# Kernel optimization log

Hardware: AMD Instinct MI355X
Metric: run time of the kernel (lower is better)

The kernel has to match this reference:

```python
import jax, jax.numpy as jnp
import numpy as np

B, S, HID = 1, 2048, 2048
NUM_HEADS, NUM_KV_HEADS, HEAD_DIM = 16, 4, 128
ROPE_THETA = 10000.0
EPS = 1e-6


def setup_inputs() -> dict:
    key = jax.random.key(0)
    ks = jax.random.split(key, 9)
    s = 0.02
    return {
        "hidden_states": jax.random.normal(ks[0], (B, S, HID), jnp.float32),
        "mu_prev": jax.random.normal(ks[1], (B, S, HID), jnp.float32),
        "wq": jax.random.normal(ks[2], (NUM_HEADS * HEAD_DIM, HID), jnp.float32) * s,
        "wk": jax.random.normal(ks[3], (NUM_KV_HEADS * HEAD_DIM, HID), jnp.float32) * s,
        "wv": jax.random.normal(ks[4], (NUM_KV_HEADS * HEAD_DIM, HID), jnp.float32) * s,
        "wo": jax.random.normal(ks[5], (HID, NUM_HEADS * HEAD_DIM), jnp.float32) * s,
        "wmq": jax.random.normal(ks[6], (NUM_HEADS * HEAD_DIM, HID), jnp.float32) * (s * 0.1),
        "wmk": jax.random.normal(ks[7], (NUM_KV_HEADS * HEAD_DIM, HID), jnp.float32) * (s * 0.1),
        "wmv": jax.random.normal(ks[8], (NUM_KV_HEADS * HEAD_DIM, HID), jnp.float32) * (s * 0.1),
        "q_norm_w": jnp.ones((HEAD_DIM,), jnp.float32),
        "k_norm_w": jnp.ones((HEAD_DIM,), jnp.float32),
    }


def _rmsnorm(x, w):
    var = jnp.mean(jnp.square(x), axis=-1, keepdims=True)
    return x * jax.lax.rsqrt(var + EPS) * w


def _rope_cos_sin(seq_len, dtype):
    inv_freq = 1.0 / (ROPE_THETA ** (jnp.arange(0, HEAD_DIM, 2, dtype=jnp.float32) / HEAD_DIM))
    freqs = jnp.arange(seq_len, dtype=jnp.float32)[:, None] * inv_freq[None, :]  # [S, D/2]
    emb = jnp.concatenate([freqs, freqs], axis=-1)  # [S, D]
    return jnp.cos(emb).astype(dtype), jnp.sin(emb).astype(dtype)


def _rotate_half(x):
    x1, x2 = jnp.split(x, 2, axis=-1)
    return jnp.concatenate([-x2, x1], axis=-1)


def reference(hidden_states, mu_prev, wq, wk, wv, wo, wmq, wmk, wmv, q_norm_w, k_norm_w):
    b, s, _ = hidden_states.shape
    # Fused mu-guided QKV projections (cat(x, mu) @ cat(W, Wm)^T == x@W^T + mu@Wm^T)
    q = hidden_states @ wq.T + mu_prev @ wmq.T  # [B,S,H*D]
    k = hidden_states @ wk.T + mu_prev @ wmk.T  # [B,S,KV*D]
    v = hidden_states @ wv.T + mu_prev @ wmv.T
    q = q.reshape(b, s, NUM_HEADS, HEAD_DIM).transpose(0, 2, 1, 3)      # [B,H,S,D]
    k = k.reshape(b, s, NUM_KV_HEADS, HEAD_DIM).transpose(0, 2, 1, 3)   # [B,KV,S,D]
    v = v.reshape(b, s, NUM_KV_HEADS, HEAD_DIM).transpose(0, 2, 1, 3)
    # per-head QK RMSNorm
    q = _rmsnorm(q, q_norm_w)
    k = _rmsnorm(k, k_norm_w)
    # RoPE
    cos, sin = _rope_cos_sin(s, q.dtype)
    q = q * cos + _rotate_half(q) * sin
    k = k * cos + _rotate_half(k) * sin
    # GQA attention without materializing repeated K/V: group query heads
    g = NUM_HEADS // NUM_KV_HEADS
    qg = q.reshape(b, NUM_KV_HEADS, g, s, HEAD_DIM)
    scale = 1.0 / jnp.sqrt(jnp.asarray(HEAD_DIM, q.dtype))
    scores = jnp.einsum('bkgqd,bkld->bkgql', qg, k) * scale  # [B,KV,G,S,S]
    causal = jnp.tril(jnp.ones((s, s), bool))
    scores = jnp.where(causal, scores, jnp.asarray(-jnp.inf, scores.dtype))
    probs = jax.nn.softmax(scores.astype(jnp.float32), axis=-1).astype(q.dtype)
    out = jnp.einsum('bkgql,bkld->bkgqd', probs, v)  # [B,KV,G,S,D]
    out = out.reshape(b, NUM_HEADS, s, HEAD_DIM).transpose(0, 2, 1, 3).reshape(b, s, NUM_HEADS * HEAD_DIM)
    return out @ wo.T
```

## Files before the change

kernel.cpp:

```cpp
#include <hip/hip_runtime.h>
#include <math.h>

#define SEQ 2048
#define HID_DIM 2048
#define NH 16
#define NKV 4
#define HD 128
#define QS 3072

typedef float  f4v  __attribute__((ext_vector_type(4)));
typedef __bf16 bf8v __attribute__((ext_vector_type(8)));
typedef __bf16 bf4v __attribute__((ext_vector_type(4)));
typedef __bf16 bf2v __attribute__((ext_vector_type(2)));

typedef __attribute__((address_space(1))) const void* gvp;
typedef __attribute__((address_space(3))) void*       svp;

__device__ __forceinline__ void gld16(const void* g, void* lds_wave_base) {
    __builtin_amdgcn_global_load_lds((gvp)g, (svp)lds_wave_base, 16, 0, 0);
}

__device__ __forceinline__ void wgb() {
    asm volatile("" ::: "memory");
    __builtin_amdgcn_s_barrier();
    asm volatile("" ::: "memory");
}
#define VMC(n) asm volatile("s_waitcnt vmcnt(" #n ")" ::: "memory")

__global__ __launch_bounds__(256)
void cvt_cat2(__bf16* __restrict__ dst, const float* __restrict__ s0,
              const float* __restrict__ s1, int rows, int kq)
{
    int i = blockIdx.x * 256 + threadIdx.x;
    if (i >= rows * kq * 2) return;
    int row = i / (2 * kq), c = i - row * 2 * kq;
    const float* s = (c < kq) ? s0 + ((size_t)row * kq + c) * 4
                              : s1 + ((size_t)row * kq + (c - kq)) * 4;
    float4 v = *reinterpret_cast<const float4*>(s);
    *reinterpret_cast<bf4v*>(dst + ((size_t)row * 2 * kq + c) * 4) =
        bf4v{ (__bf16)v.x, (__bf16)v.y, (__bf16)v.z, (__bf16)v.w };
}

__global__ __launch_bounds__(256)
void cvt(__bf16* __restrict__ dst, const float* __restrict__ src, int n4)
{
    int i = blockIdx.x * 256 + threadIdx.x;
    if (i >= n4) return;
    float4 v = *reinterpret_cast<const float4*>(src + (size_t)i * 4);
    *reinterpret_cast<bf4v*>(dst + (size_t)i * 4) =
        bf4v{ (__bf16)v.x, (__bf16)v.y, (__bf16)v.z, (__bf16)v.w };
}

__device__ __forceinline__ void stage_half(
    const __bf16* __restrict__ g, int ldk, int row0, int ktile, int half,
    char* buf, int w, int sr, int sc)
{
#pragma unroll
    for (int j = 0; j < 2; ++j) {
        int sid = w * 2 + j;
        int rb = half * 8 + (sid >> 1), cb = sid & 1;
        gld16(g + (size_t)(row0 + rb * 16 + sr) * ldk + ktile * 64 + cb * 32 + sc,
              buf + (rb * 2 + cb) * 1024);
    }
}
__device__ __forceinline__ void stage_tile(
    const __bf16* __restrict__ g, int ldk, int row0, int ktile,
    char* buf, int w, int sr, int sc)
{
    stage_half(g, ldk, row0, ktile, 0, buf, w, sr, sc);
    stage_half(g, ldk, row0, ktile, 1, buf, w, sr, sc);
}

#define LOAD_AF(DST, BUF, MTB) \
    _Pragma("unroll") for (int mt = 0; mt < 4; ++mt) \
    _Pragma("unroll") for (int ks = 0; ks < 2; ++ks) \
        DST[mt][ks] = *(const bf8v*)((BUF) + (((wm * 8 + (MTB) + mt) * 2 + ks) << 10) + frag_off);
#define LOAD_BF(DST, BUF, NTB) \
    _Pragma("unroll") for (int nt = 0; nt < 2; ++nt) \
    _Pragma("unroll") for (int ks = 0; ks < 2; ++ks) \
        DST[nt][ks] = *(const bf8v*)((BUF) + (((wn * 4 + (NTB) + nt) * 2 + ks) << 10) + frag_off);
#define MFMA_Q(MTB, NTB, AR, BR) \
    __builtin_amdgcn_s_setprio(1); \
    _Pragma("unroll") for (int mt = 0; mt < 4; ++mt) \
    _Pragma("unroll") for (int nt = 0; nt < 2; ++nt) \
    _Pragma("unroll") for (int ks = 0; ks < 2; ++ks) \
        acc[(MTB) + mt][(NTB) + nt] = __builtin_amdgcn_mfma_f32_16x16x32_bf16( \
            AR[mt][ks], BR[nt][ks], acc[(MTB) + mt][(NTB) + nt], 0, 0, 0); \
    __builtin_amdgcn_s_setprio(0);

__global__ __launch_bounds__(512, 2)
void gemm_nt_pl(const __bf16* __restrict__ A, const __bf16* __restrict__ B,
                __bf16* __restrict__ P, int M, int N, int K, int KS)
{
    __shared__ __align__(1024) char lds[131072];
    char* A0 = lds;
    char* A1 = lds + 32768;
    char* B0 = lds + 65536;
    char* B1 = lds + 98304;

    const int tid = threadIdx.x, lane = tid & 63, w = tid >> 6;
    const int wm = w >> 2, wn = w & 3;
    const int mm = lane & 15, quad = lane >> 4;
    const int m0 = blockIdx.y * 256, n0 = blockIdx.x * 256;
    const int kt0 = (blockIdx.z * KS) >> 6;
    const int T = KS >> 6;

    const int sr = lane >> 2, sc = (lane & 3) * 8;
    const int frag_off = (mm * 4 + quad) << 4;

    f4v acc[8][4] = {};
    bf8v aLo[4][2], aHi[4][2], b01e[2][2], b01o[2][2], b23[2][2];

    stage_tile(A, K, m0, kt0,     A0, w, sr, sc);
    stage_tile(B, K, n0, kt0,     B0, w, sr, sc);
    stage_tile(A, K, m0, kt0 + 1, A1, w, sr, sc);
    stage_tile(B, K, n0, kt0 + 1, B1, w, sr, sc);
    VMC(8);
    wgb();
    LOAD_AF(aLo, A0, 0)
    LOAD_BF(b01e, B0, 0)

    const int nbody = (T - 2) >> 1;
    for (int it = 0; it < nbody; ++it) {
        const int t2 = kt0 + 2 * it + 2, t3 = t2 + 1;
        LOAD_BF(b23, B0, 2)
        MFMA_Q(0, 0, aLo, b01e)
        wgb();
        LOAD_AF(aHi, A0, 4)
        MFMA_Q(0, 2, aLo, b23)
        VMC(0);
        wgb();
        LOAD_AF(aLo, A1, 0)
        stage_tile(B, K, n0, t2, B0, w, sr, sc);
        MFMA_Q(4, 2, aHi, b23)
        wgb();
        LOAD_BF(b01o, B1, 0)
        stage_tile(A, K, m0, t2, A0, w, sr, sc);
        MFMA_Q(4, 0, aHi, b01e)
        wgb();
        LOAD_BF(b23, B1, 2)
        MFMA_Q(0, 0, aLo, b01o)
        wgb();
        LOAD_AF(aHi, A1, 4)
        MFMA_Q(0, 2, aLo, b23)
        VMC(0);
        wgb();
        LOAD_AF(aLo, A0, 0)
        stage_tile(B, K, n0, t3, B1, w, sr, sc);
        MFMA_Q(4, 2, aHi, b23)
        wgb();
        LOAD_BF(b01e, B0, 0)
        stage_tile(A, K, m0, t3, A1, w, sr, sc);
        MFMA_Q(4, 0, aHi, b01o)
        wgb();
    }
    LOAD_BF(b23, B0, 2)
    MFMA_Q(0, 0, aLo, b01e)
    wgb();
    LOAD_AF(aHi, A0, 4)
    MFMA_Q(0, 2, aLo, b23)
    VMC(0);
    wgb();
    LOAD_AF(aLo, A1, 0)
    MFMA_Q(4, 2, aHi, b23)
    wgb();
    LOAD_BF(b01o, B1, 0)
    MFMA_Q(4, 0, aHi, b01e)
    wgb();
    LOAD_BF(b23, B1, 2)
    MFMA_Q(0, 0, aLo, b01o)
    wgb();
    LOAD_AF(aHi, A1, 4)
    MFMA_Q(0, 2, aLo, b23)
    wgb();
    MFMA_Q(4, 2, aHi, b23)
    MFMA_Q(4, 0, aHi, b01o)

    __bf16* Pz = P + (size_t)blockIdx.z * M * N;
#pragma unroll
    for (int mt = 0; mt < 8; ++mt)
#pragma unroll
        for (int nt = 0; nt < 4; ++nt)
#pragma unroll
            for (int r = 0; r < 4; ++r)
                Pz[(size_t)(m0 + wm * 128 + mt * 16 + quad * 4 + r) * N
                   + n0 + wn * 64 + nt * 16 + mm] = (__bf16)acc[mt][nt][r];
}

__global__ __launch_bounds__(256)
void add4(const __bf16* __restrict__ P, float* __restrict__ out, int n4)
{
    int i = blockIdx.x * 256 + threadIdx.x;
    if (i >= n4) return;
    float4 s = {0.f, 0.f, 0.f, 0.f};
#pragma unroll
    for (int z = 0; z < 4; ++z) {
        bf4v v = *reinterpret_cast<const bf4v*>(P + (size_t)z * n4 * 4 + (size_t)i * 4);
        s.x += (float)v[0]; s.y += (float)v[1]; s.z += (float)v[2]; s.w += (float)v[3];
    }
    *reinterpret_cast<float4*>(out + (size_t)i * 4) = s;
}

__global__ __launch_bounds__(64)
void norm_rope(__bf16* __restrict__ qkv ,
               const __bf16* __restrict__ p1,
               const float* __restrict__ qw, const float* __restrict__ kw)
{
    const int s = blockIdx.x, hh = blockIdx.y, l = threadIdx.x;
    const float* wn; float scale; int off;
    if (hh < NH) { off = hh * HD;               wn = qw; scale = 0.08838834764831845f; }
    else         { off = 2048 + (hh - NH) * HD; wn = kw; scale = 1.0f; }
    __bf16* p = qkv + (size_t)s * QS + off;
    const __bf16* q1 = p1 + (size_t)s * QS + off;
    float x0 = (float)p[l]      + (float)q1[l];
    float x1 = (float)p[l + 64] + (float)q1[l + 64];
    float ss = x0 * x0 + x1 * x1;
#pragma unroll
    for (int o = 32; o; o >>= 1) ss += __shfl_xor(ss, o);
    float inv = rsqrtf(ss * (1.0f / 128.0f) + 1e-6f);
    x0 *= inv * wn[l];
    x1 *= inv * wn[l + 64];
    float invf = exp2f(-(float)l * (13.287712379549449f / 64.0f));
    float ang  = (float)s * invf;
    float c, sn;
    sincosf(ang, &sn, &c);
    p[l]      = (__bf16)((x0 * c - x1 * sn) * scale);
    p[l + 64] = (__bf16)((x1 * c + x0 * sn) * scale);
}

__global__ __launch_bounds__(256)
void pack_k(const __bf16* __restrict__ qkv, __bf16* __restrict__ Kt)
{
    const int kt = blockIdx.x, kh = blockIdx.y, t = threadIdx.x;
    char* tile = (char*)Kt + ((size_t)(kh * 32 + kt)) * 16384;
    const __bf16* src = qkv + 2048 + kh * HD;
#pragma unroll
    for (int i = 0; i < 4; ++i) {
        int cid = t * 4 + i;
        int key = cid >> 4, pc = cid & 15;
        int c = pc ^ (key & 15);
        bf8v v = *reinterpret_cast<const bf8v*>(src + (size_t)(kt * 64 + key) * QS + c * 8);
        *reinterpret_cast<bf8v*>(tile + cid * 16) = v;
    }
}

__global__ __launch_bounds__(256)
void pack_v(const __bf16* __restrict__ qkv0, const __bf16* __restrict__ qkv1,
            __bf16* __restrict__ Vt)
{
    const int kt = blockIdx.x, kh = blockIdx.y, t = threadIdx.x;
    char* tile = (char*)Vt + ((size_t)(kh * 32 + kt)) * 16384;
    const __bf16* s0 = qkv0 + 2560 + kh * HD;
    const __bf16* s1 = qkv1 + 2560 + kh * HD;
#pragma unroll
    for (int i = 0; i < 4; ++i) {
        int cid = t * 4 + i;
        int d = cid >> 3, kcp = cid & 7;
        int kc = kcp ^ (d & 7);
        size_t base = (size_t)(kt * 64 + kc * 8) * QS + d;
        __bf16 tmp[8];
#pragma unroll
        for (int j = 0; j < 8; ++j)
            tmp[j] = (__bf16)((float)s0[base + (size_t)j * QS] +
                              (float)s1[base + (size_t)j * QS]);
        *reinterpret_cast<bf8v*>(tile + cid * 16) = *reinterpret_cast<bf8v*>(tmp);
    }
}

__global__ __launch_bounds__(256)
void attn_split(const __bf16* __restrict__ qkv,
                const __bf16* __restrict__ Kt, const __bf16* __restrict__ Vt,
                __bf16* __restrict__ Op, float* __restrict__ Lp)
{
    __shared__ char Ks[16384];
    __shared__ char Vs[16384];
    __shared__ char Ps[4][2048];

    const int c = blockIdx.x, qt = 31 - blockIdx.y, h = blockIdx.z;
    if (c * 8 > qt) return;
    const int kend = min(qt, c * 8 + 7);
    const int tid = threadIdx.x, lane = tid & 63, w = tid >> 6;
    const int mm = lane & 15, quad = lane >> 4;
    const int kh = h >> 2;

    bf8v aq[4];
    const __bf16* qbase = qkv + (size_t)(qt * 64 + w * 16 + mm) * QS + h * HD;
#pragma unroll
    for (int ks = 0; ks < 4; ++ks)
        aq[ks] = *reinterpret_cast<const bf8v*>(qbase + ks * 32 + quad * 8);

    float lp[4] = {};
    f4v oacc[8] = {};

    for (int kt = c * 8; kt <= kend; ++kt) {
        __syncthreads();
        const char* ktile = (const char*)Kt + ((size_t)(kh * 32 + kt)) * 16384;
        const char* vtile = (const char*)Vt + ((size_t)(kh * 32 + kt)) * 16384;
#pragma unroll
        for (int j = 0; j < 4; ++j) {
            int chunk = w * 4 + j;
            gld16(ktile + chunk * 1024 + lane * 16, Ks + chunk * 1024);
            gld16(vtile + chunk * 1024 + lane * 16, Vs + chunk * 1024);
        }
        __syncthreads();

        f4v s[4] = {};
#pragma unroll
        for (int ks = 0; ks < 4; ++ks)
#pragma unroll
            for (int c16 = 0; c16 < 4; ++c16) {
                bf8v b = *reinterpret_cast<const bf8v*>(
                    Ks + (c16 * 16 + mm) * 256 + (((ks * 4 + quad) ^ mm) << 4));
                s[c16] = __builtin_amdgcn_mfma_f32_16x16x32_bf16(aq[ks], b, s[c16], 0, 0, 0);
            }
        if (kt == qt) {
#pragma unroll
            for (int c16 = 0; c16 < 4; ++c16)
#pragma unroll
                for (int r = 0; r < 4; ++r)
                    if (c16 * 16 + mm > w * 16 + quad * 4 + r)
                        s[c16][r] = -__builtin_inff();
        }
        float pr[4][4];
#pragma unroll
        for (int c16 = 0; c16 < 4; ++c16)
#pragma unroll
            for (int r = 0; r < 4; ++r) {
                pr[c16][r] = __expf(s[c16][r]);
                lp[r] += pr[c16][r];
            }
#pragma unroll
        for (int c16 = 0; c16 < 4; ++c16)
#pragma unroll
            for (int r = 0; r < 4; ++r) {
                float mine  = pr[c16][r];
                float other = __shfl_xor(mine, 1);
                if ((mm & 1) == 0) {
                    int roww = quad * 4 + r;
                    int cc   = c16 * 2 + (mm >> 3);
                    *reinterpret_cast<bf2v*>(
                        &Ps[w][roww * 128 + ((cc ^ (roww & 7)) << 4) + (mm & 7) * 2]) =
                        bf2v{ (__bf16)mine, (__bf16)other };
                }
            }
        bf8v pa[2];
#pragma unroll
        for (int kb = 0; kb < 2; ++kb)
            pa[kb] = *reinterpret_cast<const bf8v*>(
                &Ps[w][mm * 128 + (((kb * 4 + quad) ^ (mm & 7)) << 4)]);
#pragma unroll
        for (int nb = 0; nb < 8; ++nb) {
            int d = nb * 16 + mm;
#pragma unroll
            for (int kb = 0; kb < 2; ++kb) {
                bf8v bv = *reinterpret_cast<const bf8v*>(
                    Vs + d * 128 + (((kb * 4 + quad) ^ (d & 7)) << 4));
                oacc[nb] = __builtin_amdgcn_mfma_f32_16x16x32_bf16(pa[kb], bv, oacc[nb], 0, 0, 0);
            }
        }
    }
#pragma unroll
    for (int off = 1; off < 16; off <<= 1)
#pragma unroll
        for (int r = 0; r < 4; ++r) lp[r] += __shfl_xor(lp[r], off);
#pragma unroll
    for (int r = 0; r < 4; ++r) {
        int row = qt * 64 + w * 16 + quad * 4 + r;
        size_t obase = ((size_t)(c * 16 + h) * SEQ + row) * HD;
#pragma unroll
        for (int nb = 0; nb < 8; ++nb)
            Op[obase + nb * 16 + mm] = (__bf16)oacc[nb][r];
        if (mm == 0)
            Lp[(size_t)(c * 16 + h) * SEQ + row] = lp[r];
    }
}

__global__ __launch_bounds__(64)
void combine(const __bf16* __restrict__ Op, const float* __restrict__ Lp,
             __bf16* __restrict__ ab)
{
    const int row = blockIdx.x, h = blockIdx.y, l = threadIdx.x;
    const int nch = (row >> 9) + 1;
    float L = 0.f, a0 = 0.f, a1 = 0.f;
    for (int c = 0; c < nch; ++c) {
        L += Lp[(size_t)(c * 16 + h) * SEQ + row];
        bf2v p = *reinterpret_cast<const bf2v*>(
            Op + ((size_t)(c * 16 + h) * SEQ + row) * HD + 2 * l);
        a0 += (float)p[0];
        a1 += (float)p[1];
    }
    float inv = 1.f / L;
    *reinterpret_cast<bf2v*>(ab + (size_t)row * (NH * HD) + h * HD + 2 * l) =
        bf2v{ (__bf16)(a0 * inv), (__bf16)(a1 * inv) };
}

extern "C" void kernel_launch(void* const* d_in, const int* in_sizes, int n_in,
                              void* d_out, int out_size, void* d_ws, size_t ws_size,
                              hipStream_t stream)
{
    const float* hs  = (const float*)d_in[0];
    const float* mu  = (const float*)d_in[1];
    const float* wq  = (const float*)d_in[2];
    const float* wk  = (const float*)d_in[3];
    const float* wv  = (const float*)d_in[4];
    const float* wo  = (const float*)d_in[5];
    const float* wmq = (const float*)d_in[6];
    const float* wmk = (const float*)d_in[7];
    const float* wmv = (const float*)d_in[8];
    const float* qw  = (const float*)d_in[9];
    const float* kw  = (const float*)d_in[10];
    float* out = (float*)d_out;

    char* ws = (char*)d_ws;
    __bf16* Wcat = (__bf16*)(ws + 0);
    __bf16* Acat = (__bf16*)(ws + 25165824);
    __bf16* Wo   = (__bf16*)(ws + 41943040);
    __bf16* qkvp = (__bf16*)(ws + 50331648);
    __bf16* ab   = (__bf16*)(ws + 75497472);
    __bf16* Ktl  = (__bf16*)(ws + 0);
    __bf16* Vtl  = (__bf16*)(ws + 2097152);
    __bf16* Opart= (__bf16*)(ws + 4194304);
    float*  Lpart= (float*) (ws + 37748736);
    __bf16* outp = (__bf16*)(ws + 0);

    cvt_cat2<<<dim3((2048 * 1024 + 255) / 256), 256, 0, stream>>>(Acat, hs, mu, 2048, 512);
    cvt_cat2<<<dim3((2048 * 1024 + 255) / 256), 256, 0, stream>>>(Wcat, wq, wmq, 2048, 512);
    cvt_cat2<<<dim3((512 * 1024 + 255) / 256), 256, 0, stream>>>(Wcat + (size_t)2048 * 4096, wk, wmk, 512, 512);
    cvt_cat2<<<dim3((512 * 1024 + 255) / 256), 256, 0, stream>>>(Wcat + (size_t)2560 * 4096, wv, wmv, 512, 512);
    cvt<<<dim3((1024 * 1024 + 255) / 256), 256, 0, stream>>>(Wo, wo, 1024 * 1024);

    gemm_nt_pl<<<dim3(QS / 256, SEQ / 256, 2), 512, 0, stream>>>(Acat, Wcat, qkvp, SEQ, QS, 2 * HID_DIM, HID_DIM);
    norm_rope<<<dim3(SEQ, NH + NKV), dim3(64), 0, stream>>>(qkvp, qkvp + (size_t)SEQ * QS, qw, kw);
    pack_k<<<dim3(32, NKV), 256, 0, stream>>>(qkvp, Ktl);
    pack_v<<<dim3(32, NKV), 256, 0, stream>>>(qkvp, qkvp + (size_t)SEQ * QS, Vtl);
    attn_split<<<dim3(4, 32, NH), 256, 0, stream>>>(qkvp, Ktl, Vtl, Opart, Lpart);
    combine<<<dim3(SEQ, NH), 64, 0, stream>>>(Opart, Lpart, ab);
    gemm_nt_pl<<<dim3(HID_DIM / 256, SEQ / 256, 4), 512, 0, stream>>>(ab, Wo, outp, SEQ, HID_DIM, NH * HD, 512);
    add4<<<dim3((1024 * 1024 + 255) / 256), 256, 0, stream>>>(outp, out, 1024 * 1024);
}
```

Measured before the change: 355.2 us.

## Double-buffer K/V tiles in split attention and raise MFMA wave priority

```diff
diff --git a/kernel.cpp b/kernel.cpp
--- a/kernel.cpp
+++ b/kernel.cpp
@@ -272,8 +272,8 @@
                 const __bf16* __restrict__ Kt, const __bf16* __restrict__ Vt,
                 __bf16* __restrict__ Op, float* __restrict__ Lp)
 {
-    __shared__ char Ks[16384];
-    __shared__ char Vs[16384];
+    __shared__ char Ks[2][16384];
+    __shared__ char Vs[2][16384];
     __shared__ char Ps[4][2048];
 
     const int c = blockIdx.x, qt = 31 - blockIdx.y, h = blockIdx.z;
@@ -292,27 +292,46 @@
     float lp[4] = {};
     f4v oacc[8] = {};
 
+    const char* kbase = (const char*)Kt + (size_t)(kh * 32) * 16384;
+    const char* vbase = (const char*)Vt + (size_t)(kh * 32) * 16384;
+
+#pragma unroll
+    for (int j = 0; j < 4; ++j) {
+        int chunk = w * 4 + j;
+        gld16(kbase + (size_t)(c * 8) * 16384 + chunk * 1024 + lane * 16,
+              Ks[0] + chunk * 1024);
+        gld16(vbase + (size_t)(c * 8) * 16384 + chunk * 1024 + lane * 16,
+              Vs[0] + chunk * 1024);
+    }
+
     for (int kt = c * 8; kt <= kend; ++kt) {
-        __syncthreads();
-        const char* ktile = (const char*)Kt + ((size_t)(kh * 32 + kt)) * 16384;
-        const char* vtile = (const char*)Vt + ((size_t)(kh * 32 + kt)) * 16384;
-#pragma unroll
-        for (int j = 0; j < 4; ++j) {
-            int chunk = w * 4 + j;
-            gld16(ktile + chunk * 1024 + lane * 16, Ks + chunk * 1024);
-            gld16(vtile + chunk * 1024 + lane * 16, Vs + chunk * 1024);
+        const int cur = kt & 1;
+        if (kt < kend) {
+#pragma unroll
+            for (int j = 0; j < 4; ++j) {
+                int chunk = w * 4 + j;
+                gld16(kbase + (size_t)(kt + 1) * 16384 + chunk * 1024 + lane * 16,
+                      Ks[cur ^ 1] + chunk * 1024);
+                gld16(vbase + (size_t)(kt + 1) * 16384 + chunk * 1024 + lane * 16,
+                      Vs[cur ^ 1] + chunk * 1024);
+            }
+            VMC(8);
+        } else {
+            VMC(0);
         }
-        __syncthreads();
+        wgb();
 
         f4v s[4] = {};
+        __builtin_amdgcn_s_setprio(1);
 #pragma unroll
         for (int ks = 0; ks < 4; ++ks)
 #pragma unroll
             for (int c16 = 0; c16 < 4; ++c16) {
                 bf8v b = *reinterpret_cast<const bf8v*>(
-                    Ks + (c16 * 16 + mm) * 256 + (((ks * 4 + quad) ^ mm) << 4));
+                    Ks[cur] + (c16 * 16 + mm) * 256 + (((ks * 4 + quad) ^ mm) << 4));
                 s[c16] = __builtin_amdgcn_mfma_f32_16x16x32_bf16(aq[ks], b, s[c16], 0, 0, 0);
             }
+        __builtin_amdgcn_s_setprio(0);
         if (kt == qt) {
 #pragma unroll
             for (int c16 = 0; c16 < 4; ++c16)
@@ -348,16 +367,19 @@
         for (int kb = 0; kb < 2; ++kb)
             pa[kb] = *reinterpret_cast<const bf8v*>(
                 &Ps[w][mm * 128 + (((kb * 4 + quad) ^ (mm & 7)) << 4)]);
+        __builtin_amdgcn_s_setprio(1);
 #pragma unroll
         for (int nb = 0; nb < 8; ++nb) {
             int d = nb * 16 + mm;
 #pragma unroll
             for (int kb = 0; kb < 2; ++kb) {
                 bf8v bv = *reinterpret_cast<const bf8v*>(
-                    Vs + d * 128 + (((kb * 4 + quad) ^ (d & 7)) << 4));
+                    Vs[cur] + d * 128 + (((kb * 4 + quad) ^ (d & 7)) << 4));
                 oacc[nb] = __builtin_amdgcn_mfma_f32_16x16x32_bf16(pa[kb], bv, oacc[nb], 0, 0, 0);
             }
         }
+        __builtin_amdgcn_s_setprio(0);
+        wgb();
     }
 #pragma unroll
     for (int off = 1; off < 16; off <<= 1)
```

Result: slower. 368.3 us (+3.7%).

## Retile split attention to 128-row query tiles with 8 waves and 128-key blocks

Applied to the files above, without the earlier changes.

```diff
diff --git a/kernel.cpp b/kernel.cpp
--- a/kernel.cpp
+++ b/kernel.cpp
@@ -267,16 +267,16 @@
     }
 }
 
-__global__ __launch_bounds__(256)
+__global__ __launch_bounds__(512)
 void attn_split(const __bf16* __restrict__ qkv,
                 const __bf16* __restrict__ Kt, const __bf16* __restrict__ Vt,
                 __bf16* __restrict__ Op, float* __restrict__ Lp)
 {
-    __shared__ char Ks[16384];
-    __shared__ char Vs[16384];
-    __shared__ char Ps[4][2048];
-
-    const int c = blockIdx.x, qt = 31 - blockIdx.y, h = blockIdx.z;
+    __shared__ char Ks[32768];
+    __shared__ char Vs[32768];
+    __shared__ char Ps[8][2048];
+
+    const int c = blockIdx.x, qt = 15 - blockIdx.y, h = blockIdx.z;
     if (c * 8 > qt) return;
     const int kend = min(qt, c * 8 + 7);
     const int tid = threadIdx.x, lane = tid & 63, w = tid >> 6;
@@ -284,7 +284,7 @@
     const int kh = h >> 2;
 
     bf8v aq[4];
-    const __bf16* qbase = qkv + (size_t)(qt * 64 + w * 16 + mm) * QS + h * HD;
+    const __bf16* qbase = qkv + (size_t)(qt * 128 + w * 16 + mm) * QS + h * HD;
 #pragma unroll
     for (int ks = 0; ks < 4; ++ks)
         aq[ks] = *reinterpret_cast<const bf8v*>(qbase + ks * 32 + quad * 8);
@@ -292,71 +292,81 @@
     float lp[4] = {};
     f4v oacc[8] = {};
 
-    for (int kt = c * 8; kt <= kend; ++kt) {
-        __syncthreads();
-        const char* ktile = (const char*)Kt + ((size_t)(kh * 32 + kt)) * 16384;
-        const char* vtile = (const char*)Vt + ((size_t)(kh * 32 + kt)) * 16384;
+    const char* kbase = (const char*)Kt + (size_t)(kh * 32) * 16384;
+    const char* vbase = (const char*)Vt + (size_t)(kh * 32) * 16384;
+
+    for (int tt = c * 8; tt <= kend; ++tt) {
+        wgb();
 #pragma unroll
         for (int j = 0; j < 4; ++j) {
             int chunk = w * 4 + j;
-            gld16(ktile + chunk * 1024 + lane * 16, Ks + chunk * 1024);
-            gld16(vtile + chunk * 1024 + lane * 16, Vs + chunk * 1024);
+            gld16(kbase + (size_t)tt * 32768 + chunk * 1024 + lane * 16,
+                  Ks + chunk * 1024);
+            gld16(vbase + (size_t)tt * 32768 + chunk * 1024 + lane * 16,
+                  Vs + chunk * 1024);
         }
-        __syncthreads();
-
-        f4v s[4] = {};
-#pragma unroll
-        for (int ks = 0; ks < 4; ++ks)
-#pragma unroll
-            for (int c16 = 0; c16 < 4; ++c16) {
-                bf8v b = *reinterpret_cast<const bf8v*>(
-                    Ks + (c16 * 16 + mm) * 256 + (((ks * 4 + quad) ^ mm) << 4));
-                s[c16] = __builtin_amdgcn_mfma_f32_16x16x32_bf16(aq[ks], b, s[c16], 0, 0, 0);
+        VMC(0);
+        wgb();
+
+        const int nss = (tt == qt && w < 4) ? 1 : 2;
+        for (int ss = 0; ss < nss; ++ss) {
+            const char* Ksub = Ks + ss * 16384;
+            const char* Vsub = Vs + ss * 16384;
+
+            f4v s[4] = {};
+#pragma unroll
+            for (int ks = 0; ks < 4; ++ks)
+#pragma unroll
+                for (int c16 = 0; c16 < 4; ++c16) {
+                    bf8v b = *reinterpret_cast<const bf8v*>(
+                        Ksub + (c16 * 16 + mm) * 256 + (((ks * 4 + quad) ^ mm) << 4));
+                    s[c16] = __builtin_amdgcn_mfma_f32_16x16x32_bf16(aq[ks], b, s[c16], 0, 0, 0);
+                }
+            if (tt == qt) {
+#pragma unroll
+                for (int c16 = 0; c16 < 4; ++c16)
+#pragma unroll
+                    for (int r = 0; r < 4; ++r)
+                        if (ss * 64 + c16 * 16 + mm > w * 16 + quad * 4 + r)
+                            s[c16][r] = -__builtin_inff();
             }
-        if (kt == qt) {
+            float pr[4][4];
 #pragma unroll
             for (int c16 = 0; c16 < 4; ++c16)
 #pragma unroll
-                for (int r = 0; r < 4; ++r)
-                    if (c16 * 16 + mm > w * 16 + quad * 4 + r)
-                        s[c16][r] = -__builtin_inff();
-        }
-        float pr[4][4];
-#pragma unroll
-        for (int c16 = 0; c16 < 4; ++c16)
-#pragma unroll
-            for (int r = 0; r < 4; ++r) {
-                pr[c16][r] = __expf(s[c16][r]);
-                lp[r] += pr[c16][r];
-            }
-#pragma unroll
-        for (int c16 = 0; c16 < 4; ++c16)
-#pragma unroll
-            for (int r = 0; r < 4; ++r) {
-                float mine  = pr[c16][r];
-                float other = __shfl_xor(mine, 1);
-                if ((mm & 1) == 0) {
-                    int roww = quad * 4 + r;
-                    int cc   = c16 * 2 + (mm >> 3);
-                    *reinterpret_cast<bf2v*>(
-                        &Ps[w][roww * 128 + ((cc ^ (roww & 7)) << 4) + (mm & 7) * 2]) =
-                        bf2v{ (__bf16)mine, (__bf16)other };
+                for (int r = 0; r < 4; ++r) {
+                    pr[c16][r] = __expf(s[c16][r]);
+                    lp[r] += pr[c16][r];
+                }
+#pragma unroll
+            for (int c16 = 0; c16 < 4; ++c16)
+#pragma unroll
+                for (int r = 0; r < 4; ++r) {
+                    float mine  = pr[c16][r];
+                    float other = __shfl_xor(mine, 1);
+                    if ((mm & 1) == 0) {
+                        int roww = quad * 4 + r;
+                        int cc   = c16 * 2 + (mm >> 3);
+                        *reinterpret_cast<bf2v*>(
+                            &Ps[w][roww * 128 + ((cc ^ (roww & 7)) << 4) + (mm & 7) * 2]) =
+                            bf2v{ (__bf16)mine, (__bf16)other };
+                    }
+                }
+            bf8v pa[2];
+#pragma unroll
+            for (int kb = 0; kb < 2; ++kb)
+                pa[kb] = *reinterpret_cast<const bf8v*>(
+                    &Ps[w][mm * 128 + (((kb * 4 + quad) ^ (mm & 7)) << 4)]);
+#pragma unroll
+            for (int nb = 0; nb < 8; ++nb) {
+                int d = nb * 16 + mm;
+#pragma unroll
+                for (int kb = 0; kb < 2; ++kb) {
+                    bf8v bv = *reinterpret_cast<const bf8v*>(
+                        Vsub + d * 128 + (((kb * 4 + quad) ^ (d & 7)) << 4));
+                    oacc[nb] = __builtin_amdgcn_mfma_f32_16x16x32_bf16(pa[kb], bv, oacc[nb], 0, 0, 0);
                 }
             }
-        bf8v pa[2];
-#pragma unroll
-        for (int kb = 0; kb < 2; ++kb)
-            pa[kb] = *reinterpret_cast<const bf8v*>(
-                &Ps[w][mm * 128 + (((kb * 4 + quad) ^ (mm & 7)) << 4)]);
-#pragma unroll
-        for (int nb = 0; nb < 8; ++nb) {
-            int d = nb * 16 + mm;
-#pragma unroll
-            for (int kb = 0; kb < 2; ++kb) {
-                bf8v bv = *reinterpret_cast<const bf8v*>(
-                    Vs + d * 128 + (((kb * 4 + quad) ^ (d & 7)) << 4));
-                oacc[nb] = __builtin_amdgcn_mfma_f32_16x16x32_bf16(pa[kb], bv, oacc[nb], 0, 0, 0);
-            }
         }
     }
 #pragma unroll
@@ -365,7 +375,7 @@
         for (int r = 0; r < 4; ++r) lp[r] += __shfl_xor(lp[r], off);
 #pragma unroll
     for (int r = 0; r < 4; ++r) {
-        int row = qt * 64 + w * 16 + quad * 4 + r;
+        int row = qt * 128 + w * 16 + quad * 4 + r;
         size_t obase = ((size_t)(c * 16 + h) * SEQ + row) * HD;
 #pragma unroll
         for (int nb = 0; nb < 8; ++nb)
@@ -380,7 +390,7 @@
              __bf16* __restrict__ ab)
 {
     const int row = blockIdx.x, h = blockIdx.y, l = threadIdx.x;
-    const int nch = (row >> 9) + 1;
+    const int nch = (row >> 10) + 1;
     float L = 0.f, a0 = 0.f, a1 = 0.f;
     for (int c = 0; c < nch; ++c) {
         L += Lp[(size_t)(c * 16 + h) * SEQ + row];
@@ -433,7 +443,7 @@
     norm_rope<<<dim3(SEQ, NH + NKV), dim3(64), 0, stream>>>(qkvp, qkvp + (size_t)SEQ * QS, qw, kw);
     pack_k<<<dim3(32, NKV), 256, 0, stream>>>(qkvp, Ktl);
     pack_v<<<dim3(32, NKV), 256, 0, stream>>>(qkvp, qkvp + (size_t)SEQ * QS, Vtl);
-    attn_split<<<dim3(4, 32, NH), 256, 0, stream>>>(qkvp, Ktl, Vtl, Opart, Lpart);
+    attn_split<<<dim3(2, 16, NH), 512, 0, stream>>>(qkvp, Ktl, Vtl, Opart, Lpart);
     combine<<<dim3(SEQ, NH), 64, 0, stream>>>(Opart, Lpart, ab);
     gemm_nt_pl<<<dim3(HID_DIM / 256, SEQ / 256, 4), 512, 0, stream>>>(ab, Wo, outp, SEQ, HID_DIM, NH * HD, 512);
     add4<<<dim3((1024 * 1024 + 255) / 256), 256, 0, stream>>>(outp, out, 1024 * 1024);
```

Measured after the change: 340.8 us. 4.0% less time.
